# Kernel optimization log

Measured on AMD Instinct MI355X. Metric: run time of the kernel, lower is better.

## Reference

```python
import jax, jax.numpy as jnp
import numpy as np

N_HEADS = 16

def setup_inputs() -> dict:
    key = jax.random.key(0)
    k1, k2, k3 = jax.random.split(key, 3)
    B, S, D = 4, 2048, 1024
    x = jax.random.normal(k1, (B, S, D), dtype=jnp.float32)
    w_in = jax.random.normal(k2, (D, 3 * D), dtype=jnp.float32) * (1.0 / np.sqrt(D))
    b_in = jnp.zeros((3 * D,), dtype=jnp.float32)
    w_out = jax.random.normal(k3, (D, D), dtype=jnp.float32) * (1.0 / np.sqrt(D))
    b_out = jnp.zeros((D,), dtype=jnp.float32)
    return {"x": x, "w_in": w_in, "b_in": b_in, "w_out": w_out, "b_out": b_out}

def reference(x, w_in, b_in, w_out, b_out):
    B, S, D = x.shape
    H = N_HEADS
    dh = D // H
    qkv = x @ w_in + b_in                      # [B,S,3D]
    q, k, v = jnp.split(qkv, 3, axis=-1)
    # [B,S,D] -> [B,H,S,dh]
    q = q.reshape(B, S, H, dh).transpose(0, 2, 1, 3)
    k = k.reshape(B, S, H, dh).transpose(0, 2, 1, 3)
    v = v.reshape(B, S, H, dh).transpose(0, 2, 1, 3)
    scores = jnp.einsum("bhqd,bhkd->bhqk", q, k) / jnp.sqrt(jnp.float32(dh))
    causal = jnp.tril(jnp.ones((S, S), dtype=bool))  # True = keep
    scores = jnp.where(causal, scores, -jnp.inf)
    attn = jax.nn.softmax(scores, axis=-1)
    out = jnp.einsum("bhqk,bhkd->bhqd", attn, v)
    out = out.transpose(0, 2, 1, 3).reshape(B, S, D)
    out = out @ w_out + b_out
    return (out, (k, v))
```

## Files before the change

### kernel.cpp

```cpp
#include <hip/hip_runtime.h>
#include <hip/hip_bf16.h>
#include <math.h>

typedef __bf16 bf16_t;
typedef __bf16 bf16x2 __attribute__((ext_vector_type(2)));
typedef __bf16 bf16x4 __attribute__((ext_vector_type(4)));
typedef __bf16 bf16x8 __attribute__((ext_vector_type(8)));
typedef float floatx4 __attribute__((ext_vector_type(4)));
typedef unsigned short ushort4v __attribute__((ext_vector_type(4)));

#define AS1 __attribute__((address_space(1)))
#define AS3 __attribute__((address_space(3)))

#define BB 4
#define SS 2048
#define DD 1024
#define HH 16
#define DH 64
#define MM (BB * SS)

__device__ __forceinline__ void gld_lds16(const bf16_t* g, bf16_t* l) {
    __builtin_amdgcn_global_load_lds((const AS1 void*)g, (AS3 void*)l, 16, 0, 0);
}

__global__ void detect_dtype(const unsigned short* __restrict__ x, int* __restrict__ flag) {
    if (threadIdx.x == 0) {
        int hits = 0;
        for (int i = 0; i < 128; ++i) {
            int e = (x[i] >> 7) & 0xFF;
            if (e >= 144) ++hits;
        }
        *flag = (hits >= 4) ? 1 : 0;
    }
}

__global__ __launch_bounds__(256)
void convert_x(const void* __restrict__ in, bf16_t* __restrict__ out,
               const int* __restrict__ flag, int n) {
    const int i4 = (blockIdx.x * 256 + threadIdx.x) * 4;
    if (i4 >= n) return;
    if (*flag) {
        floatx4 v = ((const floatx4*)in)[i4 >> 2];
        out[i4 + 0] = (bf16_t)v[0];
        out[i4 + 1] = (bf16_t)v[1];
        out[i4 + 2] = (bf16_t)v[2];
        out[i4 + 3] = (bf16_t)v[3];
    } else {
        ((ushort4v*)out)[i4 >> 2] = ((const ushort4v*)in)[i4 >> 2];
    }
}

__global__ void convert1d(const void* __restrict__ in, bf16_t* __restrict__ out,
                          const int* __restrict__ flag, int n) {
    const int i = blockIdx.x * 256 + threadIdx.x;
    if (i >= n) return;
    out[i] = (*flag) ? (bf16_t)((const float*)in)[i] : ((const bf16_t*)in)[i];
}

__global__ void transpose_cvt(const void* __restrict__ in, bf16_t* __restrict__ out,
                              const int* __restrict__ flag, int R, int C) {
    __shared__ bf16_t tile[32][33];
    const int tx = threadIdx.x & 31;
    const int ty = threadIdx.x >> 5;
    const int r0 = blockIdx.y * 32;
    const int c0 = blockIdx.x * 32;
    if (*flag) {
        const float* fin = (const float*)in;
#pragma unroll
        for (int i = 0; i < 32; i += 8)
            tile[ty + i][tx] = (bf16_t)fin[(size_t)(r0 + ty + i) * C + (c0 + tx)];
    } else {
        const bf16_t* bin = (const bf16_t*)in;
#pragma unroll
        for (int i = 0; i < 32; i += 8)
            tile[ty + i][tx] = bin[(size_t)(r0 + ty + i) * C + (c0 + tx)];
    }
    __syncthreads();
#pragma unroll
    for (int i = 0; i < 32; i += 8)
        out[(size_t)(c0 + ty + i) * R + (r0 + tx)] = tile[tx][ty + i];
}

__global__ __launch_bounds__(256)
void vexpand(const bf16_t* __restrict__ vt, float* __restrict__ vout) {
    __shared__ float tile[32][33];
    const int tx = threadIdx.x & 31;
    const int ty = threadIdx.x >> 5;
    const int s0 = blockIdx.x * 32;
    const int d0 = blockIdx.y * 32;
    const int bh = blockIdx.z;
#pragma unroll
    for (int i = 0; i < 32; i += 8)
        tile[ty + i][tx] = (float)vt[(size_t)(bh * DH + d0 + ty + i) * SS + s0 + tx];
    __syncthreads();
#pragma unroll
    for (int i = 0; i < 32; i += 8)
        vout[((size_t)bh * SS + s0 + ty + i) * DH + d0 + tx] = tile[tx][ty + i];
}

template <int MODE>
__global__ __launch_bounds__(512, 2)
void gemm256(const bf16_t* __restrict__ A, const bf16_t* __restrict__ Bt,
             const bf16_t* __restrict__ bias,
             bf16_t* __restrict__ qout, float* __restrict__ kf,
             bf16_t* __restrict__ kb, bf16_t* __restrict__ vtp,
             float* __restrict__ outf, int nbx, int N) {
    constexpr int KK = 1024;
    constexpr int NT = KK / 64;
    __shared__ bf16_t Ah[4][128 * 64];
    __shared__ bf16_t Bh[4][128 * 64];
    const int tid = threadIdx.x;
    const int w = tid >> 6;
    const int l = tid & 63;
    const int quad = l >> 4;
    const int l16 = l & 15;
    const int wm = w & 1;
    const int wn = w >> 1;

    const int cpx = gridDim.x >> 3;
    const int wg = (blockIdx.x & 7) * cpx + (blockIdx.x >> 3);
    const int m0 = (wg / nbx) * 256;
    const int n0 = (wg % nbx) * 256;

    const int srow = w * 8 + (l >> 3);
    const int sg = (l & 7) ^ (srow & 7);
    const bf16_t* ag = A + (size_t)m0 * KK + (size_t)srow * KK + sg * 8;
    const bf16_t* bg = Bt + (size_t)n0 * KK + (size_t)srow * KK + sg * 8;
    const int dst0 = w * 512;

    auto stA = [&](int h) {
        const bf16_t* g = ag + (size_t)(h & 1) * (128 * KK) + (h >> 1) * 64;
        bf16_t* s = &Ah[h & 3][dst0];
        gld_lds16(g, s);
        gld_lds16(g + (size_t)64 * KK, s + 4096);
    };
    auto stB = [&](int h) {
        const bf16_t* g = bg + (size_t)(h & 1) * (128 * KK) + (h >> 1) * 64;
        bf16_t* s = &Bh[h & 3][dst0];
        gld_lds16(g, s);
        gld_lds16(g + (size_t)64 * KK, s + 4096);
    };

    const int axor = l16 & 7;
    auto rdA = [&](int slot, int m, int kh) -> bf16x8 {
        return *(const bf16x8*)&Ah[slot][(m * 16 + l16) * 64 +
                                         ((((kh << 2) | quad) ^ axor) << 3)];
    };
    auto rdB = [&](int slot, int n, int kh) -> bf16x8 {
        return *(const bf16x8*)&Bh[slot][((wn & 1) * 64 + n * 16 + l16) * 64 +
                                         ((((kh << 2) | quad) ^ axor) << 3)];
    };

    floatx4 acc[8][4];
#pragma unroll
    for (int i = 0; i < 8; ++i)
#pragma unroll
        for (int j = 0; j < 4; ++j) {
            floatx4 z = {0.f, 0.f, 0.f, 0.f};
            acc[i][j] = z;
        }

    stB(0); stB(1); stA(0); stA(1); stB(2); stB(3);
    asm volatile("s_waitcnt vmcnt(4)" ::: "memory");
    __builtin_amdgcn_s_barrier();

    bf16x8 bfr[4][2];
    for (int u = 0; u < NT; ++u) {
        const int sa = (2 * u + wm) & 3;
        const int sb = (2 * u + (wn >> 1)) & 3;
#pragma unroll
        for (int p = 0; p < 4; ++p) {
            bf16x8 a00 = rdA(sa, 2 * p, 0),     a01 = rdA(sa, 2 * p, 1);
            bf16x8 a10 = rdA(sa, 2 * p + 1, 0), a11 = rdA(sa, 2 * p + 1, 1);
            if (p == 0) {
#pragma unroll
                for (int n = 0; n < 4; ++n) {
                    bfr[n][0] = rdB(sb, n, 0);
                    bfr[n][1] = rdB(sb, n, 1);
                }
            }
            if (p == 0 && u + 1 < NT) { stA(2 * u + 2); stA(2 * u + 3); }
            if (p == 2 && u + 2 < NT) stB(2 * u + 4);
            if (p == 3 && u + 2 < NT) stB(2 * u + 5);
            __builtin_amdgcn_s_barrier();
            asm volatile("s_waitcnt lgkmcnt(0)" ::: "memory");
            __builtin_amdgcn_s_setprio(1);
#pragma unroll
            for (int n = 0; n < 4; ++n) {
                acc[2 * p][n] = __builtin_amdgcn_mfma_f32_16x16x32_bf16(
                    a00, bfr[n][0], acc[2 * p][n], 0, 0, 0);
                acc[2 * p][n] = __builtin_amdgcn_mfma_f32_16x16x32_bf16(
                    a01, bfr[n][1], acc[2 * p][n], 0, 0, 0);
                acc[2 * p + 1][n] = __builtin_amdgcn_mfma_f32_16x16x32_bf16(
                    a10, bfr[n][0], acc[2 * p + 1][n], 0, 0, 0);
                acc[2 * p + 1][n] = __builtin_amdgcn_mfma_f32_16x16x32_bf16(
                    a11, bfr[n][1], acc[2 * p + 1][n], 0, 0, 0);
            }
            __builtin_amdgcn_s_setprio(0);
            if (p == 3 && u + 1 < NT) {
                if (u + 2 < NT) asm volatile("s_waitcnt vmcnt(4)" ::: "memory");
                else            asm volatile("s_waitcnt vmcnt(0)" ::: "memory");
            }
            __builtin_amdgcn_s_barrier();
        }
    }

    const int nb = n0 + wn * 64;
    const int mrow0 = m0 + wm * 128;
    float bv[4];
#pragma unroll
    for (int nt = 0; nt < 4; ++nt) bv[nt] = (float)bias[nb + nt * 16 + l16];

    if (MODE == 0) {
        const int sec = nb >> 10;
        const int c = nb & 1023;
        const int hh = c >> 6;
        const int b = mrow0 >> 11;
        const int sb0 = mrow0 & 2047;
        if (sec == 2) {
#pragma unroll
            for (int mt = 0; mt < 8; ++mt)
#pragma unroll
                for (int nt = 0; nt < 4; ++nt) {
                    const int dcol = nt * 16 + l16;
                    const int sbase = sb0 + mt * 16 + quad * 4;
                    bf16x4 pk;
#pragma unroll
                    for (int r = 0; r < 4; ++r) pk[r] = (bf16_t)(acc[mt][nt][r] + bv[nt]);
                    *(bf16x4*)&vtp[((size_t)(b * HH + hh) * DH + dcol) * SS + sbase] = pk;
                }
        } else if (sec == 0) {
#pragma unroll
            for (int mt = 0; mt < 8; ++mt)
#pragma unroll
                for (int nt = 0; nt < 4; ++nt) {
                    const int dcol = nt * 16 + l16;
#pragma unroll
                    for (int r = 0; r < 4; ++r) {
                        const int s = sb0 + mt * 16 + quad * 4 + r;
                        qout[((size_t)(b * HH + hh) * SS + s) * DH + dcol] =
                            (bf16_t)(acc[mt][nt][r] + bv[nt]);
                    }
                }
        } else {
#pragma unroll
            for (int mt = 0; mt < 8; ++mt)
#pragma unroll
                for (int nt = 0; nt < 4; ++nt) {
                    const int dcol = nt * 16 + l16;
#pragma unroll
                    for (int r = 0; r < 4; ++r) {
                        const int s = sb0 + mt * 16 + quad * 4 + r;
                        const size_t di = ((size_t)(b * HH + hh) * SS + s) * DH + dcol;
                        const float val = acc[mt][nt][r] + bv[nt];
                        kf[di] = val;
                        kb[di] = (bf16_t)val;
                    }
                }
        }
    } else {
#pragma unroll
        for (int mt = 0; mt < 8; ++mt)
#pragma unroll
            for (int nt = 0; nt < 4; ++nt)
#pragma unroll
                for (int r = 0; r < 4; ++r) {
                    const int m = mrow0 + mt * 16 + quad * 4 + r;
                    outf[(size_t)m * N + nb + nt * 16 + l16] = acc[mt][nt][r] + bv[nt];
                }
    }
}

#define PST 72

__device__ __forceinline__ void stage_kv(const bf16_t* __restrict__ g, int rstride_e,
                                         bf16_t* l, int tid, int wave) {
#pragma unroll
    for (int half = 0; half < 2; ++half) {
        const int row = half * 32 + (tid >> 3);
        const int srcslot = (tid & 7) ^ (row & 7);
        gld_lds16(g + (size_t)row * rstride_e + srcslot * 8,
                  l + half * 2048 + wave * 512);
    }
}

__device__ __forceinline__ bf16x8 ldsfrag(const bf16_t* base, int row, int s) {
    return *(const bf16x8*)&base[row * 64 + ((s ^ (row & 7)) << 3)];
}

__global__ __launch_bounds__(256)
void flash_v5(const bf16_t* __restrict__ q, const bf16_t* __restrict__ kbf,
              const bf16_t* __restrict__ vt, bf16_t* __restrict__ ao) {
    __shared__ bf16_t Ks[2][64 * 64];
    __shared__ bf16_t Vs[64 * 64];
    __shared__ bf16_t Ps[4][16 * PST];
    const int tid = threadIdx.x;
    const int wave = tid >> 6;
    const int lane = tid & 63;
    const int quad = lane >> 4;
    const int l16 = lane & 15;

    const int linear = blockIdx.x;
    const int xcd = linear & 7;
    const int sl = linear >> 3;
    const int hi = sl & 7;
    const int qt = 31 - (sl >> 3);
    const int bh = xcd * 8 + hi;
    const int r0 = qt * 64 + wave * 16;
    const int b = bh >> 4;
    const int h = bh & 15;

    const bf16_t* qp = q + (size_t)bh * SS * DH;
    const bf16_t* kp = kbf + (size_t)bh * SS * DH;
    const bf16_t* vp = vt + (size_t)bh * DH * SS;
    bf16_t* ps = Ps[wave];

    bf16x8 aq0, aq1;
    {
        const bf16_t* qr = qp + (size_t)(r0 + l16) * DH + quad * 8;
        aq0 = *(const bf16x8*)qr;
        aq1 = *(const bf16x8*)(qr + 32);
    }

    floatx4 o[4];
#pragma unroll
    for (int nt = 0; nt < 4; ++nt) {
        floatx4 z = {0.f, 0.f, 0.f, 0.f};
        o[nt] = z;
    }
    float lrow[4] = {0.f, 0.f, 0.f, 0.f};

    const float c2 = 0.18033688011112042f;
    const float FB = 16.0f;
    const int nIter = qt + 1;

    stage_kv(kp, DH, Ks[0], tid, wave);
    asm volatile("s_waitcnt vmcnt(0)" ::: "memory");
    __builtin_amdgcn_s_barrier();

    int cur = 0;
    for (int it = 0; it < nIter; ++it) {
        const int j0 = it * 64;
        stage_kv(vp + j0, SS, Vs, tid, wave);
        if (it + 1 < nIter)
            stage_kv(kp + (size_t)(j0 + 64) * DH, DH, Ks[cur ^ 1], tid, wave);

        const bf16_t* Kc = Ks[cur];
        floatx4 sc[4];
#pragma unroll
        for (int cp = 0; cp < 4; ++cp) {
            const int krow = (cp >> 1) * 32 + 2 * l16 + (cp & 1);
            const bf16x8 kf0 = ldsfrag(Kc, krow, quad);
            const bf16x8 kf1 = ldsfrag(Kc, krow, 4 + quad);
            floatx4 z = {0.f, 0.f, 0.f, 0.f};
            z = __builtin_amdgcn_mfma_f32_16x16x32_bf16(aq0, kf0, z, 0, 0, 0);
            z = __builtin_amdgcn_mfma_f32_16x16x32_bf16(aq1, kf1, z, 0, 0, 0);
            sc[cp] = z;
        }

        if (it == nIter - 1) {
#pragma unroll
            for (int r = 0; r < 4; ++r) {
                const int qi = r0 + quad * 4 + r;
                float p[4];
#pragma unroll
                for (int cp = 0; cp < 4; ++cp) {
                    const int key = j0 + (cp >> 1) * 32 + 2 * l16 + (cp & 1);
                    const float e = __builtin_amdgcn_exp2f(fmaf(sc[cp][r], c2, -FB));
                    p[cp] = (key <= qi) ? e : 0.f;
                }
                lrow[r] += (p[0] + p[1]) + (p[2] + p[3]);
                const int qrow = quad * 4 + r;
                bf16x2 w0, w1;
                w0[0] = (bf16_t)p[0]; w0[1] = (bf16_t)p[1];
                w1[0] = (bf16_t)p[2]; w1[1] = (bf16_t)p[3];
                *(bf16x2*)&ps[qrow * PST + 2 * l16] = w0;
                *(bf16x2*)&ps[qrow * PST + 32 + 2 * l16] = w1;
            }
        } else {
#pragma unroll
            for (int r = 0; r < 4; ++r) {
                float p[4];
#pragma unroll
                for (int cp = 0; cp < 4; ++cp)
                    p[cp] = __builtin_amdgcn_exp2f(fmaf(sc[cp][r], c2, -FB));
                lrow[r] += (p[0] + p[1]) + (p[2] + p[3]);
                const int qrow = quad * 4 + r;
                bf16x2 w0, w1;
                w0[0] = (bf16_t)p[0]; w0[1] = (bf16_t)p[1];
                w1[0] = (bf16_t)p[2]; w1[1] = (bf16_t)p[3];
                *(bf16x2*)&ps[qrow * PST + 2 * l16] = w0;
                *(bf16x2*)&ps[qrow * PST + 32 + 2 * l16] = w1;
            }
        }
        asm volatile("s_waitcnt lgkmcnt(0)" ::: "memory");
        bf16x8 ap0 = *(const bf16x8*)&ps[l16 * PST + quad * 8];
        bf16x8 ap1 = *(const bf16x8*)&ps[l16 * PST + 32 + quad * 8];

        asm volatile("s_waitcnt vmcnt(0) lgkmcnt(0)" ::: "memory");
        __builtin_amdgcn_s_barrier();

#pragma unroll
        for (int nt = 0; nt < 4; ++nt) {
            const int vrow = nt * 16 + l16;
            const bf16x8 vf0 = ldsfrag(Vs, vrow, quad);
            const bf16x8 vf1 = ldsfrag(Vs, vrow, 4 + quad);
            o[nt] = __builtin_amdgcn_mfma_f32_16x16x32_bf16(ap0, vf0, o[nt], 0, 0, 0);
            o[nt] = __builtin_amdgcn_mfma_f32_16x16x32_bf16(ap1, vf1, o[nt], 0, 0, 0);
        }

        asm volatile("s_waitcnt lgkmcnt(0)" ::: "memory");
        __builtin_amdgcn_s_barrier();
        cur ^= 1;
    }

#pragma unroll
    for (int r = 0; r < 4; ++r) {
#pragma unroll
        for (int off = 1; off < 16; off <<= 1)
            lrow[r] += __shfl_xor(lrow[r], off);
    }
#pragma unroll
    for (int r = 0; r < 4; ++r) {
        const float inv = 1.0f / lrow[r];
        const int s = r0 + quad * 4 + r;
        bf16_t* dst = ao + ((size_t)(b * SS + s) * DD) + h * DH;
#pragma unroll
        for (int nt = 0; nt < 4; ++nt)
            dst[nt * 16 + l16] = (bf16_t)(o[nt][r] * inv);
    }
}
#undef PST

extern "C" void kernel_launch(void* const* d_in, const int* in_sizes, int n_in,
                              void* d_out, int out_size, void* d_ws, size_t ws_size,
                              hipStream_t stream) {
    const void* x_raw = nullptr;
    const void* w_in_raw = nullptr;
    const void* b_in_raw = nullptr;
    const void* w_out_raw = nullptr;
    const void* b_out_raw = nullptr;
    for (int i = 0; i < n_in; ++i) {
        switch (in_sizes[i]) {
            case 8388608: x_raw = d_in[i]; break;
            case 3145728: w_in_raw = d_in[i]; break;
            case 3072:    b_in_raw = d_in[i]; break;
            case 1048576: w_out_raw = d_in[i]; break;
            case 1024:    b_out_raw = d_in[i]; break;
            default: break;
        }
    }

    float* outf  = (float*)d_out;
    float* koutf = outf + (size_t)MM * DD;
    float* voutf = koutf + (size_t)MM * DD;

    bf16_t* q_ws = (bf16_t*)d_out;
    bf16_t* k_bf = q_ws + (size_t)MM * DD;

    char* ws = (char*)d_ws;
    int*    flag    = (int*)ws;
    bf16_t* xc      = (bf16_t*)(ws + 256);
    bf16_t* ao_ws   = xc;
    bf16_t* w_in_t  = (bf16_t*)(ws + 16777472);
    bf16_t* w_out_t = (bf16_t*)(ws + 23068928);
    bf16_t* b_in_c  = (bf16_t*)(ws + 25166080);
    bf16_t* b_out_c = (bf16_t*)(ws + 25172224);
    bf16_t* v_t     = (bf16_t*)(ws + 25174272);

    detect_dtype<<<1, 64, 0, stream>>>((const unsigned short*)x_raw, flag);

    convert_x<<<(MM * DD / 4 + 255) / 256, 256, 0, stream>>>(x_raw, xc, flag, MM * DD);
    transpose_cvt<<<dim3(3 * DD / 32, DD / 32), 256, 0, stream>>>(w_in_raw, w_in_t, flag, DD, 3 * DD);
    transpose_cvt<<<dim3(DD / 32, DD / 32), 256, 0, stream>>>(w_out_raw, w_out_t, flag, DD, DD);
    convert1d<<<(3 * DD + 255) / 256, 256, 0, stream>>>(b_in_raw, b_in_c, flag, 3 * DD);
    convert1d<<<(DD + 255) / 256, 256, 0, stream>>>(b_out_raw, b_out_c, flag, DD);

    gemm256<0><<<dim3(384), 512, 0, stream>>>(
        xc, w_in_t, b_in_c, q_ws, koutf, k_bf, v_t, nullptr, 12, 3 * DD);

    vexpand<<<dim3(SS / 32, DH / 32, BB * HH), 256, 0, stream>>>(v_t, voutf);

    flash_v5<<<dim3((SS / 64) * BB * HH), 256, 0, stream>>>(q_ws, k_bf, v_t, ao_ws);

    gemm256<1><<<dim3(128), 512, 0, stream>>>(
        ao_ws, w_out_t, b_out_c, nullptr, nullptr, nullptr, nullptr, outf, 4, DD);
}
```

Baseline: 315.4 us.

## Software-pipeline LDS A-fragment reads with MFMA in GEMM main loop

Restructures the gemm256 inner loop so A fragments for the next sub-step are read from LDS into a second register set while MFMAs run on the current set. This double-buffers registers, reduces the number of barriers per K-step, and drops the explicit lgkmcnt(0) wait before each MFMA group, so LDS read latency is hidden behind compute. It adds register pressure from the extra fragment set, and barrier placement has to stay correct for the shared-memory slot reuse.

Result: no change. 312.0 us (-1.1%).

```diff
diff --git a/kernel.cpp b/kernel.cpp
--- a/kernel.cpp
+++ b/kernel.cpp
@@ -97,6 +97,23 @@
     for (int i = 0; i < 32; i += 8)
         vout[((size_t)bh * SS + s0 + ty + i) * DH + d0 + tx] = tile[tx][ty + i];
 }
+
+#define MFMA16(MR, S)                                                          \
+    do {                                                                       \
+        __builtin_amdgcn_s_setprio(1);                                         \
+        _Pragma("unroll")                                                      \
+        for (int n = 0; n < 4; ++n) {                                          \
+            acc[(MR)][n] = __builtin_amdgcn_mfma_f32_16x16x32_bf16(            \
+                (S)[0], bfr[n][0], acc[(MR)][n], 0, 0, 0);                     \
+            acc[(MR)][n] = __builtin_amdgcn_mfma_f32_16x16x32_bf16(            \
+                (S)[1], bfr[n][1], acc[(MR)][n], 0, 0, 0);                     \
+            acc[(MR) + 1][n] = __builtin_amdgcn_mfma_f32_16x16x32_bf16(        \
+                (S)[2], bfr[n][0], acc[(MR) + 1][n], 0, 0, 0);                 \
+            acc[(MR) + 1][n] = __builtin_amdgcn_mfma_f32_16x16x32_bf16(        \
+                (S)[3], bfr[n][1], acc[(MR) + 1][n], 0, 0, 0);                 \
+        }                                                                      \
+        __builtin_amdgcn_s_setprio(0);                                         \
+    } while (0)
 
 template <int MODE>
 __global__ __launch_bounds__(512, 2)
@@ -160,49 +177,51 @@
             acc[i][j] = z;
         }
 
+    bf16x8 S0[4], S1[4], bfr[4][2];
+
+    auto readA4 = [&](bf16x8 (&S)[4], int slot, int p) {
+        S[0] = rdA(slot, 2 * p, 0);
+        S[1] = rdA(slot, 2 * p, 1);
+        S[2] = rdA(slot, 2 * p + 1, 0);
+        S[3] = rdA(slot, 2 * p + 1, 1);
+    };
+    auto readB8 = [&](int slot) {
+#pragma unroll
+        for (int n = 0; n < 4; ++n) {
+            bfr[n][0] = rdB(slot, n, 0);
+            bfr[n][1] = rdB(slot, n, 1);
+        }
+    };
+
     stB(0); stB(1); stA(0); stA(1); stB(2); stB(3);
     asm volatile("s_waitcnt vmcnt(4)" ::: "memory");
     __builtin_amdgcn_s_barrier();
-
-    bf16x8 bfr[4][2];
+    readA4(S0, wm, 0);
+
     for (int u = 0; u < NT; ++u) {
         const int sa = (2 * u + wm) & 3;
         const int sb = (2 * u + (wn >> 1)) & 3;
-#pragma unroll
-        for (int p = 0; p < 4; ++p) {
-            bf16x8 a00 = rdA(sa, 2 * p, 0),     a01 = rdA(sa, 2 * p, 1);
-            bf16x8 a10 = rdA(sa, 2 * p + 1, 0), a11 = rdA(sa, 2 * p + 1, 1);
-            if (p == 0) {
-#pragma unroll
-                for (int n = 0; n < 4; ++n) {
-                    bfr[n][0] = rdB(sb, n, 0);
-                    bfr[n][1] = rdB(sb, n, 1);
-                }
-            }
-            if (p == 0 && u + 1 < NT) { stA(2 * u + 2); stA(2 * u + 3); }
-            if (p == 2 && u + 2 < NT) stB(2 * u + 4);
-            if (p == 3 && u + 2 < NT) stB(2 * u + 5);
-            __builtin_amdgcn_s_barrier();
-            asm volatile("s_waitcnt lgkmcnt(0)" ::: "memory");
-            __builtin_amdgcn_s_setprio(1);
-#pragma unroll
-            for (int n = 0; n < 4; ++n) {
-                acc[2 * p][n] = __builtin_amdgcn_mfma_f32_16x16x32_bf16(
-                    a00, bfr[n][0], acc[2 * p][n], 0, 0, 0);
-                acc[2 * p][n] = __builtin_amdgcn_mfma_f32_16x16x32_bf16(
-                    a01, bfr[n][1], acc[2 * p][n], 0, 0, 0);
-                acc[2 * p + 1][n] = __builtin_amdgcn_mfma_f32_16x16x32_bf16(
-                    a10, bfr[n][0], acc[2 * p + 1][n], 0, 0, 0);
-                acc[2 * p + 1][n] = __builtin_amdgcn_mfma_f32_16x16x32_bf16(
-                    a11, bfr[n][1], acc[2 * p + 1][n], 0, 0, 0);
-            }
-            __builtin_amdgcn_s_setprio(0);
-            if (p == 3 && u + 1 < NT) {
-                if (u + 2 < NT) asm volatile("s_waitcnt vmcnt(4)" ::: "memory");
-                else            asm volatile("s_waitcnt vmcnt(0)" ::: "memory");
-            }
-            __builtin_amdgcn_s_barrier();
-        }
+        const int sa_n = (2 * u + 2 + wm) & 3;
+        if (u + 1 < NT) { stA(2 * u + 2); stA(2 * u + 3); }
+        __builtin_amdgcn_s_barrier();
+        readB8(sb);
+        readA4(S1, sa, 1);
+        MFMA16(0, S0);
+        __builtin_amdgcn_s_barrier();
+        readA4(S0, sa, 2);
+        MFMA16(2, S1);
+        if (u + 2 < NT) stB(2 * u + 4);
+        __builtin_amdgcn_s_barrier();
+        readA4(S1, sa, 3);
+        MFMA16(4, S0);
+        if (u + 2 < NT) stB(2 * u + 5);
+        if (u + 1 < NT) {
+            if (u + 2 < NT) asm volatile("s_waitcnt vmcnt(4)" ::: "memory");
+            else            asm volatile("s_waitcnt vmcnt(0)" ::: "memory");
+        }
+        __builtin_amdgcn_s_barrier();
+        if (u + 1 < NT) readA4(S0, sa_n, 0);
+        MFMA16(6, S1);
     }
 
     const int nb = n0 + wn * 64;
@@ -270,6 +289,7 @@
                 }
     }
 }
+#undef MFMA16
 
 #define PST 72
 
```

## Halve GEMM M-tile to 128 and fuse fp32 V output into QKV epilogue

Applied to the files above, without the earlier changes.

Both GEMMs now use 128x256 block tiles instead of 256x256, doubling the grid sizes to 768 and 256 blocks, with a reworked per-k-step schedule of LDS reads, MFMAs and staged loads. The separate vexpand kernel is removed, and the QKV GEMM epilogue writes the fp32 V output directly alongside the bf16 transposed V. This targets poor CU fill on the output projection, which previously had only 128 blocks, and saves one launch plus a re-read of V. The cost is lower operand reuse per block and an uncoalesced strided fp32 V store in the epilogue.

New measurement: 294.5 us. 1.07x faster.

```diff
diff --git a/kernel.cpp b/kernel.cpp
--- a/kernel.cpp
+++ b/kernel.cpp
@@ -81,22 +81,14 @@
         out[(size_t)(c0 + ty + i) * R + (r0 + tx)] = tile[tx][ty + i];
 }
 
-__global__ __launch_bounds__(256)
-void vexpand(const bf16_t* __restrict__ vt, float* __restrict__ vout) {
-    __shared__ float tile[32][33];
-    const int tx = threadIdx.x & 31;
-    const int ty = threadIdx.x >> 5;
-    const int s0 = blockIdx.x * 32;
-    const int d0 = blockIdx.y * 32;
-    const int bh = blockIdx.z;
-#pragma unroll
-    for (int i = 0; i < 32; i += 8)
-        tile[ty + i][tx] = (float)vt[(size_t)(bh * DH + d0 + ty + i) * SS + s0 + tx];
-    __syncthreads();
-#pragma unroll
-    for (int i = 0; i < 32; i += 8)
-        vout[((size_t)bh * SS + s0 + ty + i) * DH + d0 + tx] = tile[tx][ty + i];
-}
+#define MFMA8(I, AF)                                                           \
+    _Pragma("unroll")                                                          \
+    for (int n = 0; n < 4; ++n) {                                              \
+        acc[I][n] = __builtin_amdgcn_mfma_f32_16x16x32_bf16(                   \
+            AF[0], bfr[n][0], acc[I][n], 0, 0, 0);                             \
+        acc[I][n] = __builtin_amdgcn_mfma_f32_16x16x32_bf16(                   \
+            AF[1], bfr[n][1], acc[I][n], 0, 0, 0);                             \
+    }
 
 template <int MODE>
 __global__ __launch_bounds__(512, 2)
@@ -104,10 +96,11 @@
              const bf16_t* __restrict__ bias,
              bf16_t* __restrict__ qout, float* __restrict__ kf,
              bf16_t* __restrict__ kb, bf16_t* __restrict__ vtp,
-             float* __restrict__ outf, int nbx, int N) {
+             float* __restrict__ vf, float* __restrict__ outf,
+             int nbx, int N) {
     constexpr int KK = 1024;
     constexpr int NT = KK / 64;
-    __shared__ bf16_t Ah[4][128 * 64];
+    __shared__ bf16_t Ah[4][64 * 64];
     __shared__ bf16_t Bh[4][128 * 64];
     const int tid = threadIdx.x;
     const int w = tid >> 6;
@@ -119,94 +112,82 @@
 
     const int cpx = gridDim.x >> 3;
     const int wg = (blockIdx.x & 7) * cpx + (blockIdx.x >> 3);
-    const int m0 = (wg / nbx) * 256;
+    const int m0 = (wg / nbx) * 128;
     const int n0 = (wg % nbx) * 256;
 
-    const int srow = w * 8 + (l >> 3);
-    const int sg = (l & 7) ^ (srow & 7);
-    const bf16_t* ag = A + (size_t)m0 * KK + (size_t)srow * KK + sg * 8;
-    const bf16_t* bg = Bt + (size_t)n0 * KK + (size_t)srow * KK + sg * 8;
+    const int srow = tid >> 3;
+    const int sg = (tid & 7) ^ (srow & 7);
+    const bf16_t* ag = A + (size_t)(m0 + srow) * KK + sg * 8;
+    const bf16_t* bg = Bt + (size_t)(n0 + srow) * KK + sg * 8;
     const int dst0 = w * 512;
 
-    auto stA = [&](int h) {
-        const bf16_t* g = ag + (size_t)(h & 1) * (128 * KK) + (h >> 1) * 64;
-        bf16_t* s = &Ah[h & 3][dst0];
+    auto stA = [&](int u, int half) {
+        gld_lds16(ag + (size_t)half * 64 * KK + u * 64,
+                  &Ah[(2 * u + half) & 3][dst0]);
+    };
+    auto stB = [&](int u, int half) {
+        const bf16_t* g = bg + (size_t)half * 128 * KK + u * 64;
+        bf16_t* s = &Bh[(2 * u + half) & 3][dst0];
         gld_lds16(g, s);
         gld_lds16(g + (size_t)64 * KK, s + 4096);
     };
-    auto stB = [&](int h) {
-        const bf16_t* g = bg + (size_t)(h & 1) * (128 * KK) + (h >> 1) * 64;
-        bf16_t* s = &Bh[h & 3][dst0];
-        gld_lds16(g, s);
-        gld_lds16(g + (size_t)64 * KK, s + 4096);
-    };
 
     const int axor = l16 & 7;
-    auto rdA = [&](int slot, int m, int kh) -> bf16x8 {
-        return *(const bf16x8*)&Ah[slot][(m * 16 + l16) * 64 +
+    auto rdA = [&](int slot, int mt, int kh) -> bf16x8 {
+        return *(const bf16x8*)&Ah[slot][(mt * 16 + l16) * 64 +
                                          ((((kh << 2) | quad) ^ axor) << 3)];
     };
-    auto rdB = [&](int slot, int n, int kh) -> bf16x8 {
-        return *(const bf16x8*)&Bh[slot][((wn & 1) * 64 + n * 16 + l16) * 64 +
+    auto rdB = [&](int slot, int nt, int kh) -> bf16x8 {
+        return *(const bf16x8*)&Bh[slot][((wn & 1) * 64 + nt * 16 + l16) * 64 +
                                          ((((kh << 2) | quad) ^ axor) << 3)];
     };
 
-    floatx4 acc[8][4];
-#pragma unroll
-    for (int i = 0; i < 8; ++i)
+    floatx4 acc[4][4];
+#pragma unroll
+    for (int i = 0; i < 4; ++i)
 #pragma unroll
         for (int j = 0; j < 4; ++j) {
             floatx4 z = {0.f, 0.f, 0.f, 0.f};
             acc[i][j] = z;
         }
 
-    stB(0); stB(1); stA(0); stA(1); stB(2); stB(3);
+    bf16x8 bfr[4][2], a0[2], a1[2], a2[2], a3[2];
+
+    stB(0, 0); stB(0, 1); stA(0, 0); stA(0, 1); stB(1, 0); stB(1, 1);
     asm volatile("s_waitcnt vmcnt(4)" ::: "memory");
     __builtin_amdgcn_s_barrier();
 
-    bf16x8 bfr[4][2];
     for (int u = 0; u < NT; ++u) {
         const int sa = (2 * u + wm) & 3;
         const int sb = (2 * u + (wn >> 1)) & 3;
-#pragma unroll
-        for (int p = 0; p < 4; ++p) {
-            bf16x8 a00 = rdA(sa, 2 * p, 0),     a01 = rdA(sa, 2 * p, 1);
-            bf16x8 a10 = rdA(sa, 2 * p + 1, 0), a11 = rdA(sa, 2 * p + 1, 1);
-            if (p == 0) {
-#pragma unroll
-                for (int n = 0; n < 4; ++n) {
-                    bfr[n][0] = rdB(sb, n, 0);
-                    bfr[n][1] = rdB(sb, n, 1);
-                }
-            }
-            if (p == 0 && u + 1 < NT) { stA(2 * u + 2); stA(2 * u + 3); }
-            if (p == 2 && u + 2 < NT) stB(2 * u + 4);
-            if (p == 3 && u + 2 < NT) stB(2 * u + 5);
-            __builtin_amdgcn_s_barrier();
-            asm volatile("s_waitcnt lgkmcnt(0)" ::: "memory");
-            __builtin_amdgcn_s_setprio(1);
-#pragma unroll
-            for (int n = 0; n < 4; ++n) {
-                acc[2 * p][n] = __builtin_amdgcn_mfma_f32_16x16x32_bf16(
-                    a00, bfr[n][0], acc[2 * p][n], 0, 0, 0);
-                acc[2 * p][n] = __builtin_amdgcn_mfma_f32_16x16x32_bf16(
-                    a01, bfr[n][1], acc[2 * p][n], 0, 0, 0);
-                acc[2 * p + 1][n] = __builtin_amdgcn_mfma_f32_16x16x32_bf16(
-                    a10, bfr[n][0], acc[2 * p + 1][n], 0, 0, 0);
-                acc[2 * p + 1][n] = __builtin_amdgcn_mfma_f32_16x16x32_bf16(
-                    a11, bfr[n][1], acc[2 * p + 1][n], 0, 0, 0);
-            }
-            __builtin_amdgcn_s_setprio(0);
-            if (p == 3 && u + 1 < NT) {
-                if (u + 2 < NT) asm volatile("s_waitcnt vmcnt(4)" ::: "memory");
-                else            asm volatile("s_waitcnt vmcnt(0)" ::: "memory");
-            }
-            __builtin_amdgcn_s_barrier();
-        }
+        if (u + 1 < NT) { stA(u + 1, 0); stA(u + 1, 1); }
+        __builtin_amdgcn_s_barrier();
+#pragma unroll
+        for (int n = 0; n < 4; ++n) {
+            bfr[n][0] = rdB(sb, n, 0);
+            bfr[n][1] = rdB(sb, n, 1);
+        }
+        a0[0] = rdA(sa, 0, 0); a0[1] = rdA(sa, 0, 1);
+        MFMA8(0, a0);
+        __builtin_amdgcn_s_barrier();
+        a1[0] = rdA(sa, 1, 0); a1[1] = rdA(sa, 1, 1);
+        MFMA8(1, a1);
+        if (u + 2 < NT) stB(u + 2, 0);
+        __builtin_amdgcn_s_barrier();
+        a2[0] = rdA(sa, 2, 0); a2[1] = rdA(sa, 2, 1);
+        a3[0] = rdA(sa, 3, 0); a3[1] = rdA(sa, 3, 1);
+        MFMA8(2, a2);
+        if (u + 2 < NT) stB(u + 2, 1);
+        if (u + 1 < NT) {
+            if (u + 2 < NT) asm volatile("s_waitcnt vmcnt(4)" ::: "memory");
+            else            asm volatile("s_waitcnt vmcnt(0)" ::: "memory");
+        }
+        __builtin_amdgcn_s_barrier();
+        MFMA8(3, a3);
     }
 
     const int nb = n0 + wn * 64;
-    const int mrow0 = m0 + wm * 128;
+    const int mrow0 = m0 + wm * 64;
     float bv[4];
 #pragma unroll
     for (int nt = 0; nt < 4; ++nt) bv[nt] = (float)bias[nb + nt * 16 + l16];
@@ -219,19 +200,23 @@
         const int sb0 = mrow0 & 2047;
         if (sec == 2) {
 #pragma unroll
-            for (int mt = 0; mt < 8; ++mt)
+            for (int mt = 0; mt < 4; ++mt)
 #pragma unroll
                 for (int nt = 0; nt < 4; ++nt) {
                     const int dcol = nt * 16 + l16;
                     const int sbase = sb0 + mt * 16 + quad * 4;
                     bf16x4 pk;
 #pragma unroll
-                    for (int r = 0; r < 4; ++r) pk[r] = (bf16_t)(acc[mt][nt][r] + bv[nt]);
+                    for (int r = 0; r < 4; ++r) {
+                        const float val = acc[mt][nt][r] + bv[nt];
+                        pk[r] = (bf16_t)val;
+                        vf[((size_t)(b * HH + hh) * SS + sbase + r) * DH + dcol] = val;
+                    }
                     *(bf16x4*)&vtp[((size_t)(b * HH + hh) * DH + dcol) * SS + sbase] = pk;
                 }
         } else if (sec == 0) {
 #pragma unroll
-            for (int mt = 0; mt < 8; ++mt)
+            for (int mt = 0; mt < 4; ++mt)
 #pragma unroll
                 for (int nt = 0; nt < 4; ++nt) {
                     const int dcol = nt * 16 + l16;
@@ -244,7 +229,7 @@
                 }
         } else {
 #pragma unroll
-            for (int mt = 0; mt < 8; ++mt)
+            for (int mt = 0; mt < 4; ++mt)
 #pragma unroll
                 for (int nt = 0; nt < 4; ++nt) {
                     const int dcol = nt * 16 + l16;
@@ -260,7 +245,7 @@
         }
     } else {
 #pragma unroll
-        for (int mt = 0; mt < 8; ++mt)
+        for (int mt = 0; mt < 4; ++mt)
 #pragma unroll
             for (int nt = 0; nt < 4; ++nt)
 #pragma unroll
@@ -270,6 +255,7 @@
                 }
     }
 }
+#undef MFMA8
 
 #define PST 72
 
@@ -476,13 +462,12 @@
     convert1d<<<(3 * DD + 255) / 256, 256, 0, stream>>>(b_in_raw, b_in_c, flag, 3 * DD);
     convert1d<<<(DD + 255) / 256, 256, 0, stream>>>(b_out_raw, b_out_c, flag, DD);
 
-    gemm256<0><<<dim3(384), 512, 0, stream>>>(
-        xc, w_in_t, b_in_c, q_ws, koutf, k_bf, v_t, nullptr, 12, 3 * DD);
-
-    vexpand<<<dim3(SS / 32, DH / 32, BB * HH), 256, 0, stream>>>(v_t, voutf);
+    gemm256<0><<<dim3(768), 512, 0, stream>>>(
+        xc, w_in_t, b_in_c, q_ws, koutf, k_bf, v_t, voutf, nullptr, 12, 3 * DD);
 
     flash_v5<<<dim3((SS / 64) * BB * HH), 256, 0, stream>>>(q_ws, k_bf, v_t, ao_ws);
 
-    gemm256<1><<<dim3(128), 512, 0, stream>>>(
-        ao_ws, w_out_t, b_out_c, nullptr, nullptr, nullptr, nullptr, outf, 4, DD);
-}
+    gemm256<1><<<dim3(256), 512, 0, stream>>>(
+        ao_ws, w_out_t, b_out_c, nullptr, nullptr, nullptr, nullptr, nullptr,
+        outf, 4, DD);
+}
```
